# Performance work log

Measured on AMD Instinct MI355X. Metric: run time of the kernel, lower is better.

The kernel has to match this reference:

```python
import jax, jax.numpy as jnp
import numpy as np
import math

B, S, E, H = 4, 1024, 1024, 16
D = E // H
C = 1.0           # Poincare ball curvature
CS = math.sqrt(C)
EPS = 1e-7

def _sq(x):
    return jnp.sum(x * x, axis=-1, keepdims=True)

def expmap0(v):
    n = jnp.sqrt(jnp.clip(_sq(v), 1e-15))
    return jnp.tanh(CS * n) * v / (CS * n)

def logmap0(y):
    n = jnp.sqrt(jnp.clip(_sq(y), 1e-15))
    t = jnp.clip(CS * n, 0.0, 1.0 - 1e-6)
    return jnp.arctanh(t) * y / (CS * n)

def hlinear(x, z, r):
    # Poincare fully-connected layer (HNN++, Shimizu et al.), as in hypll HLinear
    lam = 2.0 / jnp.clip(1.0 - C * _sq(x), EPS)          # [..., 1] conformal factor
    zn = jnp.clip(jnp.linalg.norm(z, axis=0), 1e-15)     # [out]
    xz = x @ z                                           # [..., out]
    tcr = 2.0 * CS * r
    v = (2.0 * zn / CS) * jnp.arcsinh(CS * lam * xz / zn * jnp.cosh(tcr) - (lam - 1.0) * jnp.sinh(tcr))
    w = jnp.sinh(CS * v) / CS
    return w / (1.0 + jnp.sqrt(1.0 + C * jnp.sum(w * w, -1, keepdims=True)))

def _beta(a, b):
    return math.exp(math.lgamma(a) + math.lgamma(b) - math.lgamma(a + b))

def _forward(query, key, value, zq, bq, zk, bk, zv, bv):
    pq, pk, pv = hlinear(query, zq, bq), hlinear(key, zk, bk), hlinear(value, zv, bv)
    split = lambda x: x.reshape(B, S, H, D).transpose(0, 2, 1, 3)   # [B,H,S,D]
    q, k, v = split(pq), split(pk), split(pv)
    # attention_similarity: negative per-head pairwise Poincare distance (all heads vectorized)
    q2 = jnp.sum(q * q, -1)                              # [B,H,Sq]
    k2 = jnp.sum(k * k, -1)                              # [B,H,Sk]
    qk = jnp.einsum('bhqd,bhkd->bhqk', q, k)
    diff2 = jnp.clip(q2[..., :, None] + k2[..., None, :] - 2.0 * qk, 0.0)
    den = jnp.clip((1.0 - C * q2)[..., :, None] * (1.0 - C * k2)[..., None, :], EPS)
    dist = jnp.arccosh(jnp.clip(1.0 + 2.0 * C * diff2 / den, 1.0 + 1e-6)) / CS
    # attention_activation: softmax over keys
    w = jax.nn.softmax(-dist, axis=-1)                   # [B,H,Sq,Sk]
    # attention_midpoint: weighted gyromidpoint of values over keys
    lam = 2.0 / jnp.clip(1.0 - C * jnp.sum(v * v, -1), EPS)          # [B,H,Sk]
    num = jnp.einsum('bhqk,bhkd->bhqd', w * lam[..., None, :], v)
    dnm = jnp.clip(jnp.einsum('bhqk,bhk->bhq', jnp.abs(w), lam - 1.0), EPS)
    u = num / dnm[..., None]
    mid = u / (1.0 + jnp.sqrt(jnp.clip(1.0 - C * _sq(u), EPS)))      # (1/2) Mobius scalar mult
    # manifold.cat: beta-concatenation of heads (HNN++)
    scale = _beta(E / 2.0, 0.5) / _beta(D / 2.0, 0.5)
    tv = logmap0(mid) * scale                            # tangent at origin, [B,H,S,D]
    return expmap0(tv.transpose(0, 2, 1, 3).reshape(B, S, E))

def setup_inputs():
    key = jax.random.key(0)
    ks = jax.random.split(key, 9)
    mk = lambda k: expmap0(jax.random.normal(k, (B, S, E), jnp.float32) * (0.3 / math.sqrt(E)))
    zs = lambda k: jax.random.normal(k, (E, E), jnp.float32) / math.sqrt(E)
    bs = lambda k: jax.random.normal(k, (E,), jnp.float32) * 0.01
    return {"query": mk(ks[0]), "key": mk(ks[1]), "value": mk(ks[2]),
            "zq": zs(ks[3]), "bq": bs(ks[4]), "zk": zs(ks[5]), "bk": bs(ks[6]),
            "zv": zs(ks[7]), "bv": bs(ks[8])}

def reference(query, key, value, zq, bq, zk, bk, zv, bv):
    return _forward(query, key, value, zq, bq, zk, bk, zv, bv)
```

## Files before the change

kernel.cpp:

```cpp
#include <hip/hip_runtime.h>
#include <cmath>

#define EPSF 1e-7f

constexpr int B_ = 4, S_ = 1024, E_ = 1024, H_ = 16, D_ = 64;
constexpr int BS_ = B_ * S_;

typedef __attribute__((ext_vector_type(8))) short bf16x8;
typedef __attribute__((ext_vector_type(4))) float f32x4;

__device__ inline unsigned int fbits(float f) { union { float f; unsigned int u; } x; x.f = f; return x.u; }
__device__ inline float ubits(unsigned int u) { union { unsigned int u; float f; } x; x.u = u; return x.f; }

__device__ inline unsigned short f2bf(float f) {
  unsigned int u = fbits(f);
  unsigned int r = u + 0x7fffu + ((u >> 16) & 1u);
  return (unsigned short)(r >> 16);
}
__device__ inline float bf2f(unsigned short h) { return ubits(((unsigned int)h) << 16); }
__device__ inline float fastrcp(float x) { return __builtin_amdgcn_rcpf(x); }
__device__ inline float fastsqrt(float x) { return __builtin_amdgcn_sqrtf(x); }

__device__ __forceinline__ void async_ld16(const unsigned short* g, unsigned short* l) {
  __builtin_amdgcn_global_load_lds(
      (const __attribute__((address_space(1))) unsigned int*)g,
      (__attribute__((address_space(3))) unsigned int*)l, 16, 0, 0);
}

__device__ __forceinline__ unsigned int cvt_pk_bf16(float lo, float hi) {
  unsigned int r;
  asm("v_cvt_pk_bf16_f32 %0, %1, %2" : "=v"(r) : "v"(lo), "v"(hi));
  return r;
}
__device__ __forceinline__ void permlane32_swap(unsigned int &a, unsigned int &b) {
  asm("v_permlane32_swap_b32 %0, %1" : "+v"(a), "+v"(b));
}
__device__ __forceinline__ void permlane16_swap(unsigned int &a, unsigned int &b) {
  asm("v_permlane16_swap_b32 %0, %1" : "+v"(a), "+v"(b));
}

__global__ __launch_bounds__(256) void xsplit_kernel(
    const float* __restrict__ xq, const float* __restrict__ xk,
    const float* __restrict__ xv, unsigned short* __restrict__ Xbf,
    float* __restrict__ lamRow) {
  const int row = blockIdx.x;
  const float* x = (row < BS_) ? xq : (row < 2 * BS_ ? xk : xv);
  const int r = row & (BS_ - 1);
  const int tid = threadIdx.x;
  float4 v = ((const float4*)(x + (size_t)r * E_))[tid];
  float s = v.x * v.x + v.y * v.y + v.z * v.z + v.w * v.w;
  #pragma unroll
  for (int m = 1; m < 64; m <<= 1) s += __shfl_xor(s, m, 64);
  __shared__ float red[4];
  if ((tid & 63) == 0) red[tid >> 6] = s;
  __syncthreads();
  s = red[0] + red[1] + red[2] + red[3];
  uint2 p;
  p.x = (unsigned int)f2bf(v.x) | ((unsigned int)f2bf(v.y) << 16);
  p.y = (unsigned int)f2bf(v.z) | ((unsigned int)f2bf(v.w) << 16);
  ((uint2*)(Xbf + (size_t)row * E_))[tid] = p;
  if (tid == 0) lamRow[row] = 2.0f / fmaxf(1.0f - s, EPSF);
}

__global__ __launch_bounds__(256) void zsplit_kernel(
    const float* __restrict__ zq, const float* __restrict__ zk, const float* __restrict__ zv,
    unsigned short* __restrict__ BhiT, float* __restrict__ Zpart) {
  const int mat = blockIdx.z;
  const float* z = mat == 0 ? zq : (mat == 1 ? zk : zv);
  const int k0 = blockIdx.y * 64, n0 = blockIdx.x * 64;
  __shared__ float t[64][65];
  __shared__ float sred[64][4];
  const int tid = threadIdx.x;
  {
    int kr = tid >> 4, nc = (tid & 15) * 4;
    #pragma unroll
    for (int i = 0; i < 4; i++) {
      float4 vv = *(const float4*)(z + (size_t)(k0 + kr + i * 16) * E_ + n0 + nc);
      t[kr + i * 16][nc + 0] = vv.x;
      t[kr + i * 16][nc + 1] = vv.y;
      t[kr + i * 16][nc + 2] = vv.z;
      t[kr + i * 16][nc + 3] = vv.w;
    }
  }
  __syncthreads();
  int nr = tid >> 2, kc = (tid & 3) * 16;
  unsigned int ph[8];
  float ss = 0.f;
  #pragma unroll
  for (int p = 0; p < 8; p++) {
    float x0 = t[kc + 2 * p][nr], x1 = t[kc + 2 * p + 1][nr];
    ph[p] = (unsigned int)f2bf(x0) | ((unsigned int)f2bf(x1) << 16);
    ss += x0 * x0 + x1 * x1;
  }
  size_t off = (size_t)mat * E_ * E_ + (size_t)(n0 + nr) * E_ + k0 + kc;
  uint4* dh = (uint4*)(BhiT + off);
  dh[0] = make_uint4(ph[0], ph[1], ph[2], ph[3]);
  dh[1] = make_uint4(ph[4], ph[5], ph[6], ph[7]);
  sred[nr][tid & 3] = ss;
  __syncthreads();
  if (tid < 64) {
    float v = sred[tid][0] + sred[tid][1] + sred[tid][2] + sred[tid][3];
    Zpart[(size_t)(mat * 16 + blockIdx.y) * E_ + n0 + tid] = v;
  }
}

__global__ __launch_bounds__(256) void zstat_final_kernel(
    const float* __restrict__ Zpart,
    const float* __restrict__ bq, const float* __restrict__ bk, const float* __restrict__ bv,
    float* __restrict__ znA, float* __restrict__ chA, float* __restrict__ shA) {
  const int idx = blockIdx.x * 256 + threadIdx.x;
  const int mat = idx >> 10, col = idx & 1023;
  const float* bb = mat == 0 ? bq : (mat == 1 ? bk : bv);
  float s = 0.f;
  #pragma unroll
  for (int ky = 0; ky < 16; ky++)
    s += Zpart[(size_t)(mat * 16 + ky) * E_ + col];
  float n = fmaxf(sqrtf(s), 1e-15f);
  znA[idx] = n;
  float rb = bb[col];
  chA[idx] = coshf(2.f * rb);
  shA[idx] = sinhf(2.f * rb);
}

__global__ __launch_bounds__(256, 3) void hlinear_mfma_kernel(
    const unsigned short* __restrict__ Xbf,
    const unsigned short* __restrict__ BhiT,
    const float* __restrict__ lamRow, const float* __restrict__ znA,
    const float* __restrict__ chA, const float* __restrict__ shA,
    unsigned short* __restrict__ Wbf) {
  const int mat = blockIdx.z;
  const unsigned short* xa = Xbf + (size_t)mat * BS_ * E_;
  const unsigned short* bh = BhiT + (size_t)mat * E_ * E_;
  const int lid = blockIdx.y * 8 + blockIdx.x;
  const int sqi = lid >> 4, offb = lid & 15;
  const int m0 = ((sqi >> 1) * 4 + (offb & 3)) * 128;
  const int n0 = ((sqi & 1) * 4 + (offb >> 2)) * 128;

  __shared__ unsigned short LDSU[18432];
  unsigned short* As = LDSU;
  unsigned short* Bh = LDSU + 8192;

  const int tid = threadIdx.x;
  const int wid = tid >> 6, lane = tid & 63, quad = lane >> 4, l16 = lane & 15;
  const int wm = (wid >> 1) * 64, wn = (wid & 1) * 64;

  f32x4 acc[4][4];
  #pragma unroll
  for (int i = 0; i < 4; i++)
    #pragma unroll
    for (int j = 0; j < 4; j++) acc[i][j] = (f32x4){0.f, 0.f, 0.f, 0.f};

  const int lrow = lane >> 3;
  const int lcs = ((lane & 7) ^ lrow) * 8;
  const int xsw = (l16 & 7);

  for (int kt = 0; kt < E_ / 64; ++kt) {
    __syncthreads();
    const int kb = kt * 64 + lcs;
    #pragma unroll
    for (int c2 = 0; c2 < 4; c2++) {
      const int c = wid * 4 + c2;
      const int grow = c * 8 + lrow;
      async_ld16(xa + (size_t)(m0 + grow) * E_ + kb, As + c * 512);
      async_ld16(bh + (size_t)(n0 + grow) * E_ + kb, Bh + c * 512);
    }
    __syncthreads();
    #pragma unroll
    for (int h = 0; h < 2; h++) {
      bf16x8 a[4];
      #pragma unroll
      for (int mt = 0; mt < 4; mt++) {
        int row = wm + mt * 16 + l16;
        a[mt] = *(const bf16x8*)&As[row * 64 + (((h * 4 + quad) ^ xsw) * 8)];
      }
      #pragma unroll
      for (int nt = 0; nt < 4; nt++) {
        int row = wn + nt * 16 + l16;
        bf16x8 bhf = *(const bf16x8*)&Bh[row * 64 + (((h * 4 + quad) ^ xsw) * 8)];
        #pragma unroll
        for (int mt = 0; mt < 4; mt++)
          acc[mt][nt] = __builtin_amdgcn_mfma_f32_16x16x32_bf16(a[mt], bhf, acc[mt][nt], 0, 0, 0);
      }
    }
  }

  const float* lamP = lamRow + mat * BS_;
  float lamv[16];
  #pragma unroll
  for (int mt = 0; mt < 4; mt++)
    #pragma unroll
    for (int r = 0; r < 4; r++)
      lamv[mt * 4 + r] = lamP[m0 + wm + mt * 16 + quad * 4 + r];

  __syncthreads();
  unsigned short* epi = LDSU + wid * 4608;
  #pragma unroll
  for (int nt = 0; nt < 4; nt++) {
    int cg = n0 + wn + nt * 16 + l16;
    float zn = znA[mat * E_ + cg];
    float chzn = chA[mat * E_ + cg] / zn;
    float sh = shA[mat * E_ + cg];
    float tzn = 2.f * zn;
    #pragma unroll
    for (int mt = 0; mt < 4; mt++) {
      #pragma unroll
      for (int r = 0; r < 4; r++) {
        float lam = lamv[mt * 4 + r];
        float arg = fmaf(lam * acc[mt][nt][r], chzn, -(lam - 1.f) * sh);
        float sq2 = sqrtf(fmaf(arg, arg, 1.f));
        float v = tzn * __logf(arg + sq2);
        float ev = __expf(v);
        float w = 0.5f * (ev - fastrcp(ev));
        epi[(mt * 16 + quad * 4 + r) * 72 + nt * 16 + l16] = f2bf(w);
      }
    }
  }
  unsigned short* gout = Wbf + (size_t)mat * BS_ * E_ + (size_t)(m0 + wm) * E_ + n0 + wn;
  const int rrow = lane >> 3, seg = lane & 7;
  #pragma unroll
  for (int i = 0; i < 8; i++) {
    int row = i * 8 + rrow;
    uint4 val = *(const uint4*)&epi[row * 72 + seg * 8];
    *(uint4*)(gout + (size_t)row * E_ + seg * 8) = val;
  }
}

__global__ __launch_bounds__(256) void normalize_kernel(
    const unsigned short* __restrict__ Wbf, unsigned short* __restrict__ Pbf,
    float* __restrict__ HN) {
  const unsigned short* w = Wbf + (size_t)blockIdx.x * E_;
  int tid = threadIdx.x;
  uint2 wv = ((const uint2*)w)[tid];
  float w0 = bf2f((unsigned short)(wv.x & 0xFFFF));
  float w1 = bf2f((unsigned short)(wv.x >> 16));
  float w2 = bf2f((unsigned short)(wv.y & 0xFFFF));
  float w3 = bf2f((unsigned short)(wv.y >> 16));
  float s = w0 * w0 + w1 * w1 + w2 * w2 + w3 * w3;
  #pragma unroll
  for (int m = 1; m < 64; m <<= 1) s += __shfl_xor(s, m, 64);
  __shared__ float red[4];
  if ((tid & 63) == 0) red[tid >> 6] = s;
  __syncthreads();
  s = red[0] + red[1] + red[2] + red[3];
  float t = 1.f / (1.f + sqrtf(1.f + s));
  unsigned short p0 = f2bf(w0 * t), p1 = f2bf(w1 * t), p2 = f2bf(w2 * t), p3 = f2bf(w3 * t);
  uint2 pk;
  pk.x = (unsigned int)p0 | ((unsigned int)p1 << 16);
  pk.y = (unsigned int)p2 | ((unsigned int)p3 << 16);
  ((uint2*)(Pbf + (size_t)blockIdx.x * E_))[tid] = pk;
  float r0 = bf2f(p0), r1 = bf2f(p1), r2 = bf2f(p2), r3 = bf2f(p3);
  float hs = r0 * r0 + r1 * r1 + r2 * r2 + r3 * r3;
  hs += __shfl_xor(hs, 1, 64);
  hs += __shfl_xor(hs, 2, 64);
  hs += __shfl_xor(hs, 4, 64);
  hs += __shfl_xor(hs, 8, 64);
  if ((tid & 15) == 0) HN[(size_t)blockIdx.x * H_ + (tid >> 4)] = hs;
}

__global__ __launch_bounds__(256) void vtrans_kernel(
    const unsigned short* __restrict__ Pbf, const float* __restrict__ HN,
    unsigned short* __restrict__ KsG, unsigned short* __restrict__ VtG,
    unsigned short* __restrict__ lamMG, unsigned int* __restrict__ auxG) {
  const int st = blockIdx.x, h = blockIdx.y, b = blockIdx.z;
  const unsigned short* pk = Pbf + (size_t)BS_ * E_;
  const unsigned short* pv = Pbf + (size_t)2 * BS_ * E_;
  const float* hnk = HN + (size_t)BS_ * H_;
  const float* hnv = HN + (size_t)2 * BS_ * H_;
  __shared__ unsigned short T[64][72];
  __shared__ float lamS[64], cS[64];
  const int tid = threadIdx.x;
  const size_t bhS = (size_t)(b * H_ + h) * S_;
  {
    int lr = tid >> 2, lc = (tid & 3) * 16;
    const uint4* src = (const uint4*)(pv + (size_t)(b * S_ + st * 64 + lr) * E_ + h * 64 + lc);
    *(uint4*)&T[lr][lc] = src[0];
    *(uint4*)&T[lr][lc + 8] = src[1];
  }
  if (tid < 64) {
    float v2 = hnv[(size_t)(b * S_ + st * 64 + tid) * H_ + h];
    float lam = 2.f / fmaxf(1.f - v2, EPSF);
    lamS[tid] = lam;
    size_t sidx = bhS + st * 64 + tid;
    lamMG[sidx] = f2bf(lam - 1.f);
    float k2 = hnk[(size_t)(b * S_ + st * 64 + tid) * H_ + h];
    float rc = fastrcp(1.f - k2);
    cS[tid] = rc;
    auxG[sidx] = (unsigned int)f2bf(rc) | ((unsigned int)f2bf(rc * k2) << 16);
  }
  __syncthreads();
  {
    int d = tid >> 2, sc = (tid & 3) * 16;
    unsigned int o[8];
    #pragma unroll
    for (int i = 0; i < 8; i++) {
      int s0 = sc + 2 * i;
      float f0 = bf2f(T[s0][d]) * lamS[s0];
      float f1 = bf2f(T[s0 + 1][d]) * lamS[s0 + 1];
      o[i] = (unsigned int)f2bf(f0) | ((unsigned int)f2bf(f1) << 16);
    }
    unsigned short* dst = VtG + (bhS * 64) + (size_t)d * S_ + st * 64 + sc;
    ((uint4*)dst)[0] = make_uint4(o[0], o[1], o[2], o[3]);
    ((uint4*)dst)[1] = make_uint4(o[4], o[5], o[6], o[7]);
  }
  {
    int lr = tid >> 2, lc = (tid & 3) * 16;
    float c = cS[lr];
    const uint4* src = (const uint4*)(pk + (size_t)(b * S_ + st * 64 + lr) * E_ + h * 64 + lc);
    union { uint4 q; unsigned short s[8]; } i0, i1, o0, o1;
    i0.q = src[0]; i1.q = src[1];
    #pragma unroll
    for (int j = 0; j < 8; j++) {
      o0.s[j] = f2bf(bf2f(i0.s[j]) * c);
      o1.s[j] = f2bf(bf2f(i1.s[j]) * c);
    }
    unsigned short* dst = KsG + (bhS + st * 64 + lr) * 64 + lc;
    ((uint4*)dst)[0] = o0.q;
    ((uint4*)dst)[1] = o1.q;
  }
}

__global__ __launch_bounds__(512) void attention_kernel(
    const unsigned short* __restrict__ Pbf, const float* __restrict__ HN,
    const unsigned short* __restrict__ KsG, const unsigned short* __restrict__ VtG,
    const unsigned short* __restrict__ lamMG, const unsigned int* __restrict__ auxG,
    float* __restrict__ TV, float scale) {
  const int fid = blockIdx.x;
  const int xcd = fid & 7, slot = fid >> 3;
  const int group = xcd + 8 * (slot >> 3);
  const int qt = slot & 7;
  const int h = group & 15, b = group >> 4;

  const unsigned short* pq = Pbf;
  const float* hnq = HN;

  const int tid = threadIdx.x;
  const int wid = tid >> 6, lane = tid & 63;
  const int quad = lane >> 4, l16 = lane & 15;

  __shared__ __align__(16) unsigned short Kl[3][4096];
  __shared__ __align__(16) unsigned short Vl[3][4096];
  __shared__ __align__(16) unsigned short lamL[1024];
  __shared__ __align__(16) unsigned int auxL[1024];

  const size_t bhS = (size_t)(b * H_ + h) * S_;
  const int lr = lane >> 3, cch = lane & 7;
  const int xsw = l16 & 7;
  const unsigned short* kbase = KsG + bhS * 64;
  const unsigned short* vbase = VtG + bhS * 64;
  const int srow = wid * 8 + lr;
  const int scc = ((cch ^ lr) * 8);

  async_ld16(kbase + (size_t)srow * 64 + scc, &Kl[0][wid * 512]);
  async_ld16(vbase + (size_t)srow * S_ + scc, &Vl[0][wid * 512]);
  async_ld16(kbase + (size_t)(64 + srow) * 64 + scc, &Kl[1][wid * 512]);
  async_ld16(vbase + (size_t)(srow * S_ + 64) + scc, &Vl[1][wid * 512]);

  ((unsigned int*)lamL)[tid] = ((const unsigned int*)(lamMG + bhS))[tid];
  ((uint2*)auxL)[tid] = ((const uint2*)(auxG + bhS))[tid];

  const int qrow0 = qt * 128 + wid * 16;
  const size_t qgrow = ((size_t)(b * S_ + qrow0 + l16)) * E_ + h * 64;
  bf16x8 aq0r = *(const bf16x8*)(pq + qgrow + quad * 8);
  bf16x8 aq1r = *(const bf16x8*)(pq + qgrow + 32 + quad * 8);
  const float q2l = hnq[((size_t)(b * S_ + qrow0 + l16)) * H_ + h];
  const float al = 2.f * fastrcp(1.f - q2l);
  const float sc2 = -2.f * al;
  bf16x8 aq0, aq1;
  #pragma unroll
  for (int j = 0; j < 8; j++) {
    aq0[j] = (short)f2bf(bf2f((unsigned short)aq0r[j]) * sc2);
    aq1[j] = (short)f2bf(bf2f((unsigned short)aq1r[j]) * sc2);
  }
  const unsigned short ae0 = (quad == 0) ? f2bf(al * q2l) : 0;
  const unsigned short ae1 = (quad == 0) ? f2bf(al) : 0;
  const bf16x8 aex = (bf16x8){(short)ae0, (short)ae1, 0, 0, 0, 0, 0, 0};

  f32x4 accO[4];
  #pragma unroll
  for (int dt = 0; dt < 4; dt++) accO[dt] = (f32x4){0.f, 0.f, 0.f, 0.f};
  f32x4 accD = (f32x4){0.f, 0.f, 0.f, 0.f};

  asm volatile("s_waitcnt vmcnt(0) lgkmcnt(0)" ::: "memory");
  __builtin_amdgcn_s_barrier();

  const int NT = S_ / 64;
  int cur = 0, pf = 2;
  #pragma unroll 1
  for (int kt = 0; kt < NT; ++kt) {
    if (kt + 2 < NT) {
      async_ld16(kbase + (size_t)((kt + 2) * 64 + srow) * 64 + scc, &Kl[pf][wid * 512]);
      async_ld16(vbase + (size_t)(srow * S_ + (kt + 2) * 64) + scc, &Vl[pf][wid * 512]);
    }
    const unsigned short* Kb = Kl[cur];
    const unsigned short* Vb = Vl[cur];

    unsigned int Wp[4][2];
    #pragma unroll
    for (int nt = 0; nt < 4; nt++) {
      const int krow = nt * 16 + l16;
      bf16x8 bk0 = *(const bf16x8*)&Kb[krow * 64 + ((quad ^ xsw) * 8)];
      bf16x8 bk1 = *(const bf16x8*)&Kb[krow * 64 + (((4 + quad) ^ xsw) * 8)];
      unsigned int av = (quad == 0) ? auxL[kt * 64 + krow] : 0u;
      bf16x8 bex = (bf16x8){(short)(av & 0xFFFF), (short)(av >> 16), 0, 0, 0, 0, 0, 0};
      f32x4 z = (f32x4){0.f, 0.f, 0.f, 0.f};
      f32x4 st = __builtin_amdgcn_mfma_f32_16x16x32_bf16(bex, aex, z, 0, 0, 0);
      st = __builtin_amdgcn_mfma_f32_16x16x32_bf16(bk0, aq0, st, 0, 0, 0);
      st = __builtin_amdgcn_mfma_f32_16x16x32_bf16(bk1, aq1, st, 0, 0, 0);
      float w[4];
      #pragma unroll
      for (int r2 = 0; r2 < 4; r2++) {
        float t = fmaxf(st[r2], 1e-6f);
        float A = 1.f + t;
        w[r2] = A - fastsqrt(fmaf(A, A, -1.f));
      }
      Wp[nt][0] = cvt_pk_bf16(w[0], w[1]);
      Wp[nt][1] = cvt_pk_bf16(w[2], w[3]);
    }
    unsigned int x00 = Wp[0][0], y00 = Wp[1][0];
    permlane32_swap(x00, y00); permlane16_swap(x00, y00);
    unsigned int x01 = Wp[0][1], y01 = Wp[1][1];
    permlane32_swap(x01, y01); permlane16_swap(x01, y01);
    unsigned int x10 = Wp[2][0], y10 = Wp[3][0];
    permlane32_swap(x10, y10); permlane16_swap(x10, y10);
    unsigned int x11 = Wp[2][1], y11 = Wp[3][1];
    permlane32_swap(x11, y11); permlane16_swap(x11, y11);
    union { unsigned int u[4]; bf16x8 v; } ap0u, ap1u;
    ap0u.u[0] = x00; ap0u.u[1] = x01; ap0u.u[2] = y00; ap0u.u[3] = y01;
    ap1u.u[0] = x10; ap1u.u[1] = x11; ap1u.u[2] = y10; ap1u.u[3] = y11;
    const bf16x8 ap0 = ap0u.v, ap1 = ap1u.v;

    #pragma unroll
    for (int dt = 0; dt < 4; dt++) {
      const int drow = dt * 16 + l16;
      bf16x8 bv0 = *(const bf16x8*)&Vb[drow * 64 + ((quad ^ xsw) * 8)];
      bf16x8 bv1 = *(const bf16x8*)&Vb[drow * 64 + (((4 + quad) ^ xsw) * 8)];
      accO[dt] = __builtin_amdgcn_mfma_f32_16x16x32_bf16(ap0, bv0, accO[dt], 0, 0, 0);
      accO[dt] = __builtin_amdgcn_mfma_f32_16x16x32_bf16(ap1, bv1, accO[dt], 0, 0, 0);
    }
    bf16x8 bl0 = *(const bf16x8*)&lamL[kt * 64 + quad * 8];
    bf16x8 bl1 = *(const bf16x8*)&lamL[kt * 64 + 32 + quad * 8];
    accD = __builtin_amdgcn_mfma_f32_16x16x32_bf16(ap0, bl0, accD, 0, 0, 0);
    accD = __builtin_amdgcn_mfma_f32_16x16x32_bf16(ap1, bl1, accD, 0, 0, 0);

    if (kt + 2 < NT) {
      asm volatile("s_waitcnt vmcnt(2)" ::: "memory");
    } else {
      asm volatile("s_waitcnt vmcnt(0)" ::: "memory");
    }
    __builtin_amdgcn_s_barrier();
    cur = (cur == 2) ? 0 : cur + 1;
    pf = (pf == 2) ? 0 : pf + 1;
  }

  #pragma unroll
  for (int r2 = 0; r2 < 4; r2++) {
    float rdsum = fastrcp(accD[r2]);
    float uu[4];
    float su = 0.f;
    #pragma unroll
    for (int dt = 0; dt < 4; dt++) { uu[dt] = accO[dt][r2] * rdsum; su += uu[dt] * uu[dt]; }
    su += __shfl_xor(su, 1, 64);
    su += __shfl_xor(su, 2, 64);
    su += __shfl_xor(su, 4, 64);
    su += __shfl_xor(su, 8, 64);
    float g = fastrcp(1.f + fastsqrt(fmaxf(1.f - su, EPSF)));
    float n2 = fmaxf(su * g * g, 1e-15f);
    float n = fastsqrt(n2);
    float fac = atanhf(fminf(n, 1.f - 1e-6f)) * fastrcp(n) * g * scale;
    size_t orow = ((size_t)(b * S_ + qrow0 + quad * 4 + r2)) * E_ + h * 64 + l16;
    #pragma unroll
    for (int dt = 0; dt < 4; dt++) TV[orow + dt * 16] = fac * uu[dt];
  }
}

__global__ __launch_bounds__(256) void expmap_kernel(float* __restrict__ TV) {
  float* w = TV + (size_t)blockIdx.x * E_;
  int tid = threadIdx.x;
  float4 v = ((float4*)w)[tid];
  float s = v.x * v.x + v.y * v.y + v.z * v.z + v.w * v.w;
  #pragma unroll
  for (int m = 1; m < 64; m <<= 1) s += __shfl_xor(s, m, 64);
  __shared__ float red[4];
  if ((tid & 63) == 0) red[tid >> 6] = s;
  __syncthreads();
  s = red[0] + red[1] + red[2] + red[3];
  float n = sqrtf(fmaxf(s, 1e-15f));
  float f = tanhf(n) / n;
  v.x *= f; v.y *= f; v.z *= f; v.w *= f;
  ((float4*)w)[tid] = v;
}

extern "C" void kernel_launch(void* const* d_in, const int* in_sizes, int n_in,
                              void* d_out, int out_size, void* d_ws, size_t ws_size,
                              hipStream_t stream) {
  (void)in_sizes; (void)n_in; (void)out_size; (void)ws_size;
  const float* q  = (const float*)d_in[0];
  const float* k  = (const float*)d_in[1];
  const float* v  = (const float*)d_in[2];
  const float* zq = (const float*)d_in[3];
  const float* bq = (const float*)d_in[4];
  const float* zk = (const float*)d_in[5];
  const float* bk = (const float*)d_in[6];
  const float* zv = (const float*)d_in[7];
  const float* bv = (const float*)d_in[8];

  unsigned short* Wbf = (unsigned short*)d_ws;
  unsigned short* Pbf = Wbf + (size_t)3 * BS_ * E_;
  unsigned short* BhiT = Pbf;
  unsigned short* Xbf = Pbf + (size_t)3 * BS_ * E_;
  float* HN           = (float*)(Xbf + (size_t)3 * BS_ * E_);
  float* lamRow       = HN + (size_t)3 * BS_ * H_;
  float* znA          = lamRow + 3 * BS_;
  float* chA          = znA + 3 * E_;
  float* shA          = chA + 3 * E_;
  float* Zpart        = shA + 3 * E_;
  unsigned short* VtG = (unsigned short*)(Zpart + 48 * E_);
  unsigned short* KsG = VtG + (size_t)B_ * H_ * 64 * S_;
  unsigned short* lamMG = KsG + (size_t)B_ * H_ * S_ * 64;
  unsigned int* auxG  = (unsigned int*)(lamMG + (size_t)B_ * H_ * S_);
  float* out          = (float*)d_out;

  double lb1 = lgamma(E_ / 2.0) + lgamma(0.5) - lgamma(E_ / 2.0 + 0.5);
  double lb2 = lgamma(D_ / 2.0) + lgamma(0.5) - lgamma(D_ / 2.0 + 0.5);
  float scale = (float)exp(lb1 - lb2);

  hipLaunchKernelGGL(xsplit_kernel, dim3(3 * BS_), dim3(256), 0, stream, q, k, v, Xbf, lamRow);
  hipLaunchKernelGGL(zsplit_kernel, dim3(16, 16, 3), dim3(256), 0, stream,
                     zq, zk, zv, BhiT, Zpart);
  hipLaunchKernelGGL(zstat_final_kernel, dim3(12), dim3(256), 0, stream,
                     Zpart, bq, bk, bv, znA, chA, shA);
  hipLaunchKernelGGL(hlinear_mfma_kernel, dim3(8, 32, 3), dim3(256), 0, stream,
                     Xbf, BhiT, lamRow, znA, chA, shA, Wbf);
  hipLaunchKernelGGL(normalize_kernel, dim3(3 * BS_), dim3(256), 0, stream, Wbf, Pbf, HN);
  hipLaunchKernelGGL(vtrans_kernel, dim3(16, 16, 4), dim3(256), 0, stream,
                     Pbf, HN, KsG, VtG, lamMG, auxG);
  hipLaunchKernelGGL(attention_kernel, dim3(512), dim3(512), 0, stream,
                     Pbf, HN, KsG, VtG, lamMG, auxG, out, scale);
  hipLaunchKernelGGL(expmap_kernel, dim3(BS_), dim3(256), 0, stream, out);
}
```

Measured before the change: 216.6 us.

## Merge prep kernels, fold z-stats into GEMM, wave-per-row norms, 2-stage attention buffer

Merges the x-split and z-split kernels into one launch and folds the z-column statistics into the hlinear GEMM prologue, which removes two launches. The GEMM grid is remapped so each of the 8 XCDs owns one column strip. The normalize and expmap kernels now process one row per wavefront with no LDS barrier. The attention K/V pipeline moves from a 3-deep ring of 64-key tiles to double buffering of 128-key tiles with one barrier per 128 keys, but this waits on all outstanding loads each iteration and may expose more load latency.

```diff
diff --git a/kernel.cpp b/kernel.cpp
--- a/kernel.cpp
+++ b/kernel.cpp
@@ -39,38 +39,48 @@
   asm("v_permlane16_swap_b32 %0, %1" : "+v"(a), "+v"(b));
 }
 
-__global__ __launch_bounds__(256) void xsplit_kernel(
+__global__ __launch_bounds__(256) void prep_kernel(
     const float* __restrict__ xq, const float* __restrict__ xk,
     const float* __restrict__ xv, unsigned short* __restrict__ Xbf,
-    float* __restrict__ lamRow) {
-  const int row = blockIdx.x;
-  const float* x = (row < BS_) ? xq : (row < 2 * BS_ ? xk : xv);
-  const int r = row & (BS_ - 1);
-  const int tid = threadIdx.x;
-  float4 v = ((const float4*)(x + (size_t)r * E_))[tid];
-  float s = v.x * v.x + v.y * v.y + v.z * v.z + v.w * v.w;
-  #pragma unroll
-  for (int m = 1; m < 64; m <<= 1) s += __shfl_xor(s, m, 64);
-  __shared__ float red[4];
-  if ((tid & 63) == 0) red[tid >> 6] = s;
-  __syncthreads();
-  s = red[0] + red[1] + red[2] + red[3];
-  uint2 p;
-  p.x = (unsigned int)f2bf(v.x) | ((unsigned int)f2bf(v.y) << 16);
-  p.y = (unsigned int)f2bf(v.z) | ((unsigned int)f2bf(v.w) << 16);
-  ((uint2*)(Xbf + (size_t)row * E_))[tid] = p;
-  if (tid == 0) lamRow[row] = 2.0f / fmaxf(1.0f - s, EPSF);
-}
-
-__global__ __launch_bounds__(256) void zsplit_kernel(
+    float* __restrict__ lamRow,
     const float* __restrict__ zq, const float* __restrict__ zk, const float* __restrict__ zv,
     unsigned short* __restrict__ BhiT, float* __restrict__ Zpart) {
-  const int mat = blockIdx.z;
+  const int bid = blockIdx.x;
+  const int tid = threadIdx.x;
+  if (bid < 3 * BS_ / 4) {
+    const int wid = tid >> 6, lane = tid & 63;
+    const int row = bid * 4 + wid;
+    const float* x = (row < BS_) ? xq : (row < 2 * BS_ ? xk : xv);
+    const int r = row & (BS_ - 1);
+    const float4* src = (const float4*)(x + (size_t)r * E_);
+    float4 v[4];
+    #pragma unroll
+    for (int j = 0; j < 4; j++) v[j] = src[lane + 64 * j];
+    float s = 0.f;
+    #pragma unroll
+    for (int j = 0; j < 4; j++)
+      s += v[j].x * v[j].x + v[j].y * v[j].y + v[j].z * v[j].z + v[j].w * v[j].w;
+    #pragma unroll
+    for (int m = 1; m < 64; m <<= 1) s += __shfl_xor(s, m, 64);
+    uint2* dst = (uint2*)(Xbf + (size_t)row * E_);
+    #pragma unroll
+    for (int j = 0; j < 4; j++) {
+      uint2 p;
+      p.x = (unsigned int)f2bf(v[j].x) | ((unsigned int)f2bf(v[j].y) << 16);
+      p.y = (unsigned int)f2bf(v[j].z) | ((unsigned int)f2bf(v[j].w) << 16);
+      dst[lane + 64 * j] = p;
+    }
+    if (lane == 0) lamRow[row] = 2.0f / fmaxf(1.0f - s, EPSF);
+    return;
+  }
+  const int lid = bid - 3 * BS_ / 4;
+  const int mat = lid >> 8;
+  const int rem = lid & 255;
+  const int ky = rem >> 4, nx = rem & 15;
   const float* z = mat == 0 ? zq : (mat == 1 ? zk : zv);
-  const int k0 = blockIdx.y * 64, n0 = blockIdx.x * 64;
+  const int k0 = ky * 64, n0 = nx * 64;
   __shared__ float t[64][65];
   __shared__ float sred[64][4];
-  const int tid = threadIdx.x;
   {
     int kr = tid >> 4, nc = (tid & 15) * 4;
     #pragma unroll
@@ -100,49 +110,47 @@
   __syncthreads();
   if (tid < 64) {
     float v = sred[tid][0] + sred[tid][1] + sred[tid][2] + sred[tid][3];
-    Zpart[(size_t)(mat * 16 + blockIdx.y) * E_ + n0 + tid] = v;
-  }
-}
-
-__global__ __launch_bounds__(256) void zstat_final_kernel(
-    const float* __restrict__ Zpart,
-    const float* __restrict__ bq, const float* __restrict__ bk, const float* __restrict__ bv,
-    float* __restrict__ znA, float* __restrict__ chA, float* __restrict__ shA) {
-  const int idx = blockIdx.x * 256 + threadIdx.x;
-  const int mat = idx >> 10, col = idx & 1023;
-  const float* bb = mat == 0 ? bq : (mat == 1 ? bk : bv);
-  float s = 0.f;
-  #pragma unroll
-  for (int ky = 0; ky < 16; ky++)
-    s += Zpart[(size_t)(mat * 16 + ky) * E_ + col];
-  float n = fmaxf(sqrtf(s), 1e-15f);
-  znA[idx] = n;
-  float rb = bb[col];
-  chA[idx] = coshf(2.f * rb);
-  shA[idx] = sinhf(2.f * rb);
+    Zpart[(size_t)(mat * 16 + ky) * E_ + n0 + tid] = v;
+  }
 }
 
 __global__ __launch_bounds__(256, 3) void hlinear_mfma_kernel(
     const unsigned short* __restrict__ Xbf,
     const unsigned short* __restrict__ BhiT,
-    const float* __restrict__ lamRow, const float* __restrict__ znA,
-    const float* __restrict__ chA, const float* __restrict__ shA,
+    const float* __restrict__ lamRow, const float* __restrict__ Zpart,
+    const float* __restrict__ bq, const float* __restrict__ bk, const float* __restrict__ bv,
     unsigned short* __restrict__ Wbf) {
-  const int mat = blockIdx.z;
+  const int fid = blockIdx.x;
+  const int xcd = fid & 7, rest = fid >> 3;
+  const int mat = rest >> 5;
+  const int m0 = (rest & 31) * 128;
+  const int n0 = xcd * 128;
+
   const unsigned short* xa = Xbf + (size_t)mat * BS_ * E_;
   const unsigned short* bh = BhiT + (size_t)mat * E_ * E_;
-  const int lid = blockIdx.y * 8 + blockIdx.x;
-  const int sqi = lid >> 4, offb = lid & 15;
-  const int m0 = ((sqi >> 1) * 4 + (offb & 3)) * 128;
-  const int n0 = ((sqi & 1) * 4 + (offb >> 2)) * 128;
 
   __shared__ unsigned short LDSU[18432];
+  __shared__ float chznS[128], shS[128], tznS[128];
   unsigned short* As = LDSU;
   unsigned short* Bh = LDSU + 8192;
 
   const int tid = threadIdx.x;
   const int wid = tid >> 6, lane = tid & 63, quad = lane >> 4, l16 = lane & 15;
   const int wm = (wid >> 1) * 64, wn = (wid & 1) * 64;
+
+  if (tid < 128) {
+    const int col = n0 + tid;
+    float s = 0.f;
+    #pragma unroll
+    for (int ky = 0; ky < 16; ky++)
+      s += Zpart[(size_t)(mat * 16 + ky) * E_ + col];
+    float zn = fmaxf(sqrtf(s), 1e-15f);
+    const float* bb = (mat == 0) ? bq : ((mat == 1) ? bk : bv);
+    float rb = bb[col];
+    chznS[tid] = coshf(2.f * rb) / zn;
+    shS[tid] = sinhf(2.f * rb);
+    tznS[tid] = 2.f * zn;
+  }
 
   f32x4 acc[4][4];
   #pragma unroll
@@ -196,11 +204,10 @@
   unsigned short* epi = LDSU + wid * 4608;
   #pragma unroll
   for (int nt = 0; nt < 4; nt++) {
-    int cg = n0 + wn + nt * 16 + l16;
-    float zn = znA[mat * E_ + cg];
-    float chzn = chA[mat * E_ + cg] / zn;
-    float sh = shA[mat * E_ + cg];
-    float tzn = 2.f * zn;
+    int ci = wn + nt * 16 + l16;
+    float chzn = chznS[ci];
+    float sh = shS[ci];
+    float tzn = tznS[ci];
     #pragma unroll
     for (int mt = 0; mt < 4; mt++) {
       #pragma unroll
@@ -228,33 +235,33 @@
 __global__ __launch_bounds__(256) void normalize_kernel(
     const unsigned short* __restrict__ Wbf, unsigned short* __restrict__ Pbf,
     float* __restrict__ HN) {
-  const unsigned short* w = Wbf + (size_t)blockIdx.x * E_;
-  int tid = threadIdx.x;
-  uint2 wv = ((const uint2*)w)[tid];
-  float w0 = bf2f((unsigned short)(wv.x & 0xFFFF));
-  float w1 = bf2f((unsigned short)(wv.x >> 16));
-  float w2 = bf2f((unsigned short)(wv.y & 0xFFFF));
-  float w3 = bf2f((unsigned short)(wv.y >> 16));
-  float s = w0 * w0 + w1 * w1 + w2 * w2 + w3 * w3;
+  const int wid = threadIdx.x >> 6, lane = threadIdx.x & 63;
+  const int row = blockIdx.x * 4 + wid;
+  const unsigned short* w = Wbf + (size_t)row * E_;
+  union { uint4 q[2]; unsigned short s[16]; } in;
+  in.q[0] = ((const uint4*)w)[lane * 2];
+  in.q[1] = ((const uint4*)w)[lane * 2 + 1];
+  float wv[16];
+  float s = 0.f;
+  #pragma unroll
+  for (int i = 0; i < 16; i++) { wv[i] = bf2f(in.s[i]); s += wv[i] * wv[i]; }
   #pragma unroll
   for (int m = 1; m < 64; m <<= 1) s += __shfl_xor(s, m, 64);
-  __shared__ float red[4];
-  if ((tid & 63) == 0) red[tid >> 6] = s;
-  __syncthreads();
-  s = red[0] + red[1] + red[2] + red[3];
   float t = 1.f / (1.f + sqrtf(1.f + s));
-  unsigned short p0 = f2bf(w0 * t), p1 = f2bf(w1 * t), p2 = f2bf(w2 * t), p3 = f2bf(w3 * t);
-  uint2 pk;
-  pk.x = (unsigned int)p0 | ((unsigned int)p1 << 16);
-  pk.y = (unsigned int)p2 | ((unsigned int)p3 << 16);
-  ((uint2*)(Pbf + (size_t)blockIdx.x * E_))[tid] = pk;
-  float r0 = bf2f(p0), r1 = bf2f(p1), r2 = bf2f(p2), r3 = bf2f(p3);
-  float hs = r0 * r0 + r1 * r1 + r2 * r2 + r3 * r3;
+  union { uint4 q[2]; unsigned short s[16]; } out;
+  float hs = 0.f;
+  #pragma unroll
+  for (int i = 0; i < 16; i++) {
+    unsigned short p = f2bf(wv[i] * t);
+    out.s[i] = p;
+    float r = bf2f(p);
+    hs += r * r;
+  }
+  ((uint4*)(Pbf + (size_t)row * E_))[lane * 2] = out.q[0];
+  ((uint4*)(Pbf + (size_t)row * E_))[lane * 2 + 1] = out.q[1];
   hs += __shfl_xor(hs, 1, 64);
   hs += __shfl_xor(hs, 2, 64);
-  hs += __shfl_xor(hs, 4, 64);
-  hs += __shfl_xor(hs, 8, 64);
-  if ((tid & 15) == 0) HN[(size_t)blockIdx.x * H_ + (tid >> 4)] = hs;
+  if ((lane & 3) == 0) HN[(size_t)row * H_ + (lane >> 2)] = hs;
 }
 
 __global__ __launch_bounds__(256) void vtrans_kernel(
@@ -337,8 +344,8 @@
   const int wid = tid >> 6, lane = tid & 63;
   const int quad = lane >> 4, l16 = lane & 15;
 
-  __shared__ __align__(16) unsigned short Kl[3][4096];
-  __shared__ __align__(16) unsigned short Vl[3][4096];
+  __shared__ __align__(16) unsigned short Kl[2][8192];
+  __shared__ __align__(16) unsigned short Vl[2][8192];
   __shared__ __align__(16) unsigned short lamL[1024];
   __shared__ __align__(16) unsigned int auxL[1024];
 
@@ -351,9 +358,9 @@
   const int scc = ((cch ^ lr) * 8);
 
   async_ld16(kbase + (size_t)srow * 64 + scc, &Kl[0][wid * 512]);
+  async_ld16(kbase + (size_t)(64 + srow) * 64 + scc, &Kl[0][4096 + wid * 512]);
   async_ld16(vbase + (size_t)srow * S_ + scc, &Vl[0][wid * 512]);
-  async_ld16(kbase + (size_t)(64 + srow) * 64 + scc, &Kl[1][wid * 512]);
-  async_ld16(vbase + (size_t)(srow * S_ + 64) + scc, &Vl[1][wid * 512]);
+  async_ld16(vbase + (size_t)srow * S_ + 64 + scc, &Vl[0][4096 + wid * 512]);
 
   ((unsigned int*)lamL)[tid] = ((const unsigned int*)(lamMG + bhS))[tid];
   ((uint2*)auxL)[tid] = ((const uint2*)(auxG + bhS))[tid];
@@ -383,73 +390,75 @@
   asm volatile("s_waitcnt vmcnt(0) lgkmcnt(0)" ::: "memory");
   __builtin_amdgcn_s_barrier();
 
-  const int NT = S_ / 64;
-  int cur = 0, pf = 2;
+  const int NIT = S_ / 128;
+  int buf = 0;
   #pragma unroll 1
-  for (int kt = 0; kt < NT; ++kt) {
-    if (kt + 2 < NT) {
-      async_ld16(kbase + (size_t)((kt + 2) * 64 + srow) * 64 + scc, &Kl[pf][wid * 512]);
-      async_ld16(vbase + (size_t)(srow * S_ + (kt + 2) * 64) + scc, &Vl[pf][wid * 512]);
-    }
-    const unsigned short* Kb = Kl[cur];
-    const unsigned short* Vb = Vl[cur];
-
-    unsigned int Wp[4][2];
-    #pragma unroll
-    for (int nt = 0; nt < 4; nt++) {
-      const int krow = nt * 16 + l16;
-      bf16x8 bk0 = *(const bf16x8*)&Kb[krow * 64 + ((quad ^ xsw) * 8)];
-      bf16x8 bk1 = *(const bf16x8*)&Kb[krow * 64 + (((4 + quad) ^ xsw) * 8)];
-      unsigned int av = (quad == 0) ? auxL[kt * 64 + krow] : 0u;
-      bf16x8 bex = (bf16x8){(short)(av & 0xFFFF), (short)(av >> 16), 0, 0, 0, 0, 0, 0};
-      f32x4 z = (f32x4){0.f, 0.f, 0.f, 0.f};
-      f32x4 st = __builtin_amdgcn_mfma_f32_16x16x32_bf16(bex, aex, z, 0, 0, 0);
-      st = __builtin_amdgcn_mfma_f32_16x16x32_bf16(bk0, aq0, st, 0, 0, 0);
-      st = __builtin_amdgcn_mfma_f32_16x16x32_bf16(bk1, aq1, st, 0, 0, 0);
-      float w[4];
+  for (int it = 0; it < NIT; ++it) {
+    if (it + 1 < NIT) {
+      const int kr0 = (it + 1) * 128;
+      async_ld16(kbase + (size_t)(kr0 + srow) * 64 + scc, &Kl[buf ^ 1][wid * 512]);
+      async_ld16(kbase + (size_t)(kr0 + 64 + srow) * 64 + scc, &Kl[buf ^ 1][4096 + wid * 512]);
+      async_ld16(vbase + (size_t)srow * S_ + kr0 + scc, &Vl[buf ^ 1][wid * 512]);
+      async_ld16(vbase + (size_t)srow * S_ + kr0 + 64 + scc, &Vl[buf ^ 1][4096 + wid * 512]);
+    }
+    #pragma unroll
+    for (int half = 0; half < 2; half++) {
+      const int kt = it * 2 + half;
+      const unsigned short* Kb = &Kl[buf][half * 4096];
+      const unsigned short* Vb = &Vl[buf][half * 4096];
+
+      unsigned int Wp[4][2];
       #pragma unroll
-      for (int r2 = 0; r2 < 4; r2++) {
-        float t = fmaxf(st[r2], 1e-6f);
-        float A = 1.f + t;
-        w[r2] = A - fastsqrt(fmaf(A, A, -1.f));
+      for (int nt = 0; nt < 4; nt++) {
+        const int krow = nt * 16 + l16;
+        bf16x8 bk0 = *(const bf16x8*)&Kb[krow * 64 + ((quad ^ xsw) * 8)];
+        bf16x8 bk1 = *(const bf16x8*)&Kb[krow * 64 + (((4 + quad) ^ xsw) * 8)];
+        unsigned int av = (quad == 0) ? auxL[kt * 64 + krow] : 0u;
+        bf16x8 bex = (bf16x8){(short)(av & 0xFFFF), (short)(av >> 16), 0, 0, 0, 0, 0, 0};
+        f32x4 z = (f32x4){0.f, 0.f, 0.f, 0.f};
+        f32x4 st = __builtin_amdgcn_mfma_f32_16x16x32_bf16(bex, aex, z, 0, 0, 0);
+        st = __builtin_amdgcn_mfma_f32_16x16x32_bf16(bk0, aq0, st, 0, 0, 0);
+        st = __builtin_amdgcn_mfma_f32_16x16x32_bf16(bk1, aq1, st, 0, 0, 0);
+        float w[4];
+        #pragma unroll
+        for (int r2 = 0; r2 < 4; r2++) {
+          float t = fmaxf(st[r2], 1e-6f);
+          float A = 1.f + t;
+          w[r2] = A - fastsqrt(fmaf(A, A, -1.f));
+        }
+        Wp[nt][0] = cvt_pk_bf16(w[0], w[1]);
+        Wp[nt][1] = cvt_pk_bf16(w[2], w[3]);
       }
-      Wp[nt][0] = cvt_pk_bf16(w[0], w[1]);
-      Wp[nt][1] = cvt_pk_bf16(w[2], w[3]);
-    }
-    unsigned int x00 = Wp[0][0], y00 = Wp[1][0];
-    permlane32_swap(x00, y00); permlane16_swap(x00, y00);
-    unsigned int x01 = Wp[0][1], y01 = Wp[1][1];
-    permlane32_swap(x01, y01); permlane16_swap(x01, y01);
-    unsigned int x10 = Wp[2][0], y10 = Wp[3][0];
-    permlane32_swap(x10, y10); permlane16_swap(x10, y10);
-    unsigned int x11 = Wp[2][1], y11 = Wp[3][1];
-    permlane32_swap(x11, y11); permlane16_swap(x11, y11);
-    union { unsigned int u[4]; bf16x8 v; } ap0u, ap1u;
-    ap0u.u[0] = x00; ap0u.u[1] = x01; ap0u.u[2] = y00; ap0u.u[3] = y01;
-    ap1u.u[0] = x10; ap1u.u[1] = x11; ap1u.u[2] = y10; ap1u.u[3] = y11;
-    const bf16x8 ap0 = ap0u.v, ap1 = ap1u.v;
-
-    #pragma unroll
-    for (int dt = 0; dt < 4; dt++) {
-      const int drow = dt * 16 + l16;
-      bf16x8 bv0 = *(const bf16x8*)&Vb[drow * 64 + ((quad ^ xsw) * 8)];
-      bf16x8 bv1 = *(const bf16x8*)&Vb[drow * 64 + (((4 + quad) ^ xsw) * 8)];
-      accO[dt] = __builtin_amdgcn_mfma_f32_16x16x32_bf16(ap0, bv0, accO[dt], 0, 0, 0);
-      accO[dt] = __builtin_amdgcn_mfma_f32_16x16x32_bf16(ap1, bv1, accO[dt], 0, 0, 0);
-    }
-    bf16x8 bl0 = *(const bf16x8*)&lamL[kt * 64 + quad * 8];
-    bf16x8 bl1 = *(const bf16x8*)&lamL[kt * 64 + 32 + quad * 8];
-    accD = __builtin_amdgcn_mfma_f32_16x16x32_bf16(ap0, bl0, accD, 0, 0, 0);
-    accD = __builtin_amdgcn_mfma_f32_16x16x32_bf16(ap1, bl1, accD, 0, 0, 0);
-
-    if (kt + 2 < NT) {
-      asm volatile("s_waitcnt vmcnt(2)" ::: "memory");
-    } else {
-      asm volatile("s_waitcnt vmcnt(0)" ::: "memory");
-    }
+      unsigned int x00 = Wp[0][0], y00 = Wp[1][0];
+      permlane32_swap(x00, y00); permlane16_swap(x00, y00);
+      unsigned int x01 = Wp[0][1], y01 = Wp[1][1];
+      permlane32_swap(x01, y01); permlane16_swap(x01, y01);
+      unsigned int x10 = Wp[2][0], y10 = Wp[3][0];
+      permlane32_swap(x10, y10); permlane16_swap(x10, y10);
+      unsigned int x11 = Wp[2][1], y11 = Wp[3][1];
+      permlane32_swap(x11, y11); permlane16_swap(x11, y11);
+      union { unsigned int u[4]; bf16x8 v; } ap0u, ap1u;
+      ap0u.u[0] = x00; ap0u.u[1] = x01; ap0u.u[2] = y00; ap0u.u[3] = y01;
+      ap1u.u[0] = x10; ap1u.u[1] = x11; ap1u.u[2] = y10; ap1u.u[3] = y11;
+      const bf16x8 ap0 = ap0u.v, ap1 = ap1u.v;
+
+      #pragma unroll
+      for (int dt = 0; dt < 4; dt++) {
+        const int drow = dt * 16 + l16;
+        bf16x8 bv0 = *(const bf16x8*)&Vb[drow * 64 + ((quad ^ xsw) * 8)];
+        bf16x8 bv1 = *(const bf16x8*)&Vb[drow * 64 + (((4 + quad) ^ xsw) * 8)];
+        accO[dt] = __builtin_amdgcn_mfma_f32_16x16x32_bf16(ap0, bv0, accO[dt], 0, 0, 0);
+        accO[dt] = __builtin_amdgcn_mfma_f32_16x16x32_bf16(ap1, bv1, accO[dt], 0, 0, 0);
+      }
+      bf16x8 bl0 = *(const bf16x8*)&lamL[kt * 64 + quad * 8];
+      bf16x8 bl1 = *(const bf16x8*)&lamL[kt * 64 + 32 + quad * 8];
+      accD = __builtin_amdgcn_mfma_f32_16x16x32_bf16(ap0, bl0, accD, 0, 0, 0);
+      accD = __builtin_amdgcn_mfma_f32_16x16x32_bf16(ap1, bl1, accD, 0, 0, 0);
+    }
+
+    asm volatile("s_waitcnt vmcnt(0)" ::: "memory");
     __builtin_amdgcn_s_barrier();
-    cur = (cur == 2) ? 0 : cur + 1;
-    pf = (pf == 2) ? 0 : pf + 1;
+    buf ^= 1;
   }
 
   #pragma unroll
@@ -474,20 +483,25 @@
 }
 
 __global__ __launch_bounds__(256) void expmap_kernel(float* __restrict__ TV) {
-  float* w = TV + (size_t)blockIdx.x * E_;
-  int tid = threadIdx.x;
-  float4 v = ((float4*)w)[tid];
-  float s = v.x * v.x + v.y * v.y + v.z * v.z + v.w * v.w;
+  const int wid = threadIdx.x >> 6, lane = threadIdx.x & 63;
+  const int row = blockIdx.x * 4 + wid;
+  float* w = TV + (size_t)row * E_;
+  float4 v[4];
+  #pragma unroll
+  for (int j = 0; j < 4; j++) v[j] = ((float4*)w)[lane + 64 * j];
+  float s = 0.f;
+  #pragma unroll
+  for (int j = 0; j < 4; j++)
+    s += v[j].x * v[j].x + v[j].y * v[j].y + v[j].z * v[j].z + v[j].w * v[j].w;
   #pragma unroll
   for (int m = 1; m < 64; m <<= 1) s += __shfl_xor(s, m, 64);
-  __shared__ float red[4];
-  if ((tid & 63) == 0) red[tid >> 6] = s;
-  __syncthreads();
-  s = red[0] + red[1] + red[2] + red[3];
   float n = sqrtf(fmaxf(s, 1e-15f));
   float f = tanhf(n) / n;
-  v.x *= f; v.y *= f; v.z *= f; v.w *= f;
-  ((float4*)w)[tid] = v;
+  #pragma unroll
+  for (int j = 0; j < 4; j++) {
+    v[j].x *= f; v[j].y *= f; v[j].z *= f; v[j].w *= f;
+    ((float4*)w)[lane + 64 * j] = v[j];
+  }
 }
 
 extern "C" void kernel_launch(void* const* d_in, const int* in_sizes, int n_in,
@@ -510,10 +524,7 @@
   unsigned short* Xbf = Pbf + (size_t)3 * BS_ * E_;
   float* HN           = (float*)(Xbf + (size_t)3 * BS_ * E_);
   float* lamRow       = HN + (size_t)3 * BS_ * H_;
-  float* znA          = lamRow + 3 * BS_;
-  float* chA          = znA + 3 * E_;
-  float* shA          = chA + 3 * E_;
-  float* Zpart        = shA + 3 * E_;
+  float* Zpart        = lamRow + 3 * BS_;
   unsigned short* VtG = (unsigned short*)(Zpart + 48 * E_);
   unsigned short* KsG = VtG + (size_t)B_ * H_ * 64 * S_;
   unsigned short* lamMG = KsG + (size_t)B_ * H_ * S_ * 64;
@@ -524,17 +535,14 @@
   double lb2 = lgamma(D_ / 2.0) + lgamma(0.5) - lgamma(D_ / 2.0 + 0.5);
   float scale = (float)exp(lb1 - lb2);
 
-  hipLaunchKernelGGL(xsplit_kernel, dim3(3 * BS_), dim3(256), 0, stream, q, k, v, Xbf, lamRow);
-  hipLaunchKernelGGL(zsplit_kernel, dim3(16, 16, 3), dim3(256), 0, stream,
-                     zq, zk, zv, BhiT, Zpart);
-  hipLaunchKernelGGL(zstat_final_kernel, dim3(12), dim3(256), 0, stream,
-                     Zpart, bq, bk, bv, znA, chA, shA);
-  hipLaunchKernelGGL(hlinear_mfma_kernel, dim3(8, 32, 3), dim3(256), 0, stream,
-                     Xbf, BhiT, lamRow, znA, chA, shA, Wbf);
-  hipLaunchKernelGGL(normalize_kernel, dim3(3 * BS_), dim3(256), 0, stream, Wbf, Pbf, HN);
+  hipLaunchKernelGGL(prep_kernel, dim3(3 * BS_ / 4 + 768), dim3(256), 0, stream,
+                     q, k, v, Xbf, lamRow, zq, zk, zv, BhiT, Zpart);
+  hipLaunchKernelGGL(hlinear_mfma_kernel, dim3(768), dim3(256), 0, stream,
+                     Xbf, BhiT, lamRow, Zpart, bq, bk, bv, Wbf);
+  hipLaunchKernelGGL(normalize_kernel, dim3(3 * BS_ / 4), dim3(256), 0, stream, Wbf, Pbf, HN);
   hipLaunchKernelGGL(vtrans_kernel, dim3(16, 16, 4), dim3(256), 0, stream,
                      Pbf, HN, KsG, VtG, lamMG, auxG);
   hipLaunchKernelGGL(attention_kernel, dim3(512), dim3(512), 0, stream,
                      Pbf, HN, KsG, VtG, lamMG, auxG, out, scale);
-  hipLaunchKernelGGL(expmap_kernel, dim3(BS_), dim3(256), 0, stream, out);
-}
+  hipLaunchKernelGGL(expmap_kernel, dim3(BS_ / 4), dim3(256), 0, stream, out);
+}
```

Result: no change. 219.8 us (+1.5%).
